# Kernel optimization log

Hardware: AMD Instinct MI355X
Metric: run time of the kernel (lower is better)

Reference implementation:

```python
import jax, jax.numpy as jnp
import numpy as np

B, S, HIDDEN = 1, 2048, 3584
NH, NKV, HD = 16, 8, 256
N_REP = NH // NKV
EPS = 1e-6
SCALING = 256.0 ** -0.5  # query_pre_attn_scalar=256
SOFTCAP = 50.0
NEG = -1e9


def rmsnorm(x, w):
    # Gemma RMSNorm with unit offset, computed in fp32
    xf = x.astype(jnp.float32)
    n = xf * jax.lax.rsqrt(jnp.mean(xf * xf, axis=-1, keepdims=True) + EPS)
    return (n * (1.0 + w.astype(jnp.float32))).astype(x.dtype)


def rope(x, cos, sin):
    # x: [B,S,H,D]; gemma pairs (x[:D/2], x[D/2:]) as complex (rotate-half)
    x1, x2 = jnp.split(x, 2, axis=-1)
    c = cos[None, :, None, :]
    s = sin[None, :, None, :]
    return jnp.concatenate([x1 * c - x2 * s, x1 * s + x2 * c], axis=-1).astype(x.dtype)


def setup_inputs() -> dict:
    key = jax.random.key(0)
    ks = jax.random.split(key, 6)
    hidden_states = jax.random.normal(ks[0], (B, S, HIDDEN), jnp.float32)
    w_qkv = jax.random.normal(ks[1], ((NH + 2 * NKV) * HD, HIDDEN), jnp.float32) * 0.02
    w_o = jax.random.normal(ks[2], (HIDDEN, NH * HD), jnp.float32) * 0.02
    q_norm_w = jax.random.normal(ks[3], (HD,), jnp.float32) * 0.1
    k_norm_w = jax.random.normal(ks[4], (HD,), jnp.float32) * 0.1
    k_cache = jnp.zeros((B, S, NKV, HD), jnp.float32)
    v_cache = jnp.zeros((B, S, NKV, HD), jnp.float32)
    kv_write_indices = jnp.arange(S, dtype=jnp.int32)
    # rotary tables, theta=10000
    inv_freq = 1.0 / (10000.0 ** (np.arange(0, HD, 2, dtype=np.float32) / HD))
    t = np.arange(S, dtype=np.float32)
    freqs = np.outer(t, inv_freq)  # [S, HD/2]
    cos = jnp.asarray(np.cos(freqs), jnp.float32)
    sin = jnp.asarray(np.sin(freqs), jnp.float32)
    # causal additive mask [1,1,S,S]
    causal = np.tril(np.ones((S, S), dtype=bool))
    mask = jnp.asarray(np.where(causal, 0.0, NEG).astype(np.float32))[None, None]
    return {"hidden_states": hidden_states, "cos": cos, "sin": sin,
            "kv_write_indices": kv_write_indices, "k_cache": k_cache,
            "v_cache": v_cache, "mask": mask, "w_qkv": w_qkv, "w_o": w_o,
            "q_norm_w": q_norm_w, "k_norm_w": k_norm_w}


def reference(hidden_states, cos, sin, kv_write_indices, k_cache, v_cache,
              mask, w_qkv, w_o, q_norm_w, k_norm_w):
    qkv = jnp.einsum('bsh,oh->bso', hidden_states, w_qkv)
    q_size, kv_size = NH * HD, NKV * HD
    xq = qkv[..., :q_size].reshape(B, S, NH, HD)
    xk = qkv[..., q_size:q_size + kv_size].reshape(B, S, NKV, HD)
    xv = qkv[..., q_size + kv_size:].reshape(B, S, NKV, HD)
    xq = rmsnorm(xq, q_norm_w)
    xk = rmsnorm(xk, k_norm_w)
    xq = rope(xq, cos, sin)
    xk = rope(xk, cos, sin)
    # KV cache write (index_copy_ along dim 1)
    kc = k_cache.at[:, kv_write_indices].set(xk)
    vc = v_cache.at[:, kv_write_indices].set(xv)
    # GQA expand
    key = jnp.repeat(kc, N_REP, axis=2)   # [B,S,NH,HD]
    val = jnp.repeat(vc, N_REP, axis=2)
    q = xq.transpose(0, 2, 1, 3) * SCALING  # [B,NH,S,HD]
    k = key.transpose(0, 2, 1, 3)
    v = val.transpose(0, 2, 1, 3)
    scores = jnp.einsum('bhqd,bhkd->bhqk', q, k)
    scores = jnp.tanh(scores / SOFTCAP) * SOFTCAP  # logit softcapping
    scores = scores + mask
    p = jax.nn.softmax(scores, axis=-1)
    out = jnp.einsum('bhqk,bhkd->bhqd', p, v)
    out = out.transpose(0, 2, 1, 3).reshape(B, S, NH * HD)
    return jnp.einsum('bsd,hd->bsh', out, w_o)
```

## Files before the change

kernel.cpp:

```cpp
#include <hip/hip_runtime.h>

typedef __bf16 bf16;
typedef __bf16 bf16x4 __attribute__((ext_vector_type(4)));
typedef __bf16 bf16x8 __attribute__((ext_vector_type(8)));
typedef float f32x4 __attribute__((ext_vector_type(4)));

#define S_LEN 2048
#define HID   3584
#define NHEADS 16
#define NKVH   8
#define HDIM   256
#define QKV_O  8192
#define O_IN   4096

typedef const __attribute__((address_space(1))) void* gp_t;
typedef __attribute__((address_space(3))) void* sp_t;

__device__ __forceinline__ void async16(const void* g, void* s) {
  __builtin_amdgcn_global_load_lds((gp_t)g, (sp_t)s, 16, 0, 0);
}

__device__ __forceinline__ f32x4 mfma16(bf16x8 a, bf16x8 b, f32x4 c) {
  return __builtin_amdgcn_mfma_f32_16x16x32_bf16(a, b, c, 0, 0, 0);
}

__global__ __launch_bounds__(256) void cast_kernel(const float* __restrict__ in,
                                                   bf16* __restrict__ out, int n4) {
  int i = blockIdx.x * 256 + threadIdx.x;
  if (i >= n4) return;
  f32x4 v = ((const f32x4*)in)[i];
  bf16x4 o = { (bf16)v[0], (bf16)v[1], (bf16)v[2], (bf16)v[3] };
  ((bf16x4*)out)[i] = o;
}

__global__ __launch_bounds__(256) void gemm_nt(const bf16* __restrict__ A, const bf16* __restrict__ B,
                                               float* __restrict__ C, int M, int N, int K) {
  __shared__ bf16 As[128 * 32];
  __shared__ bf16 Bs[128 * 32];
  int tid = threadIdx.x;
  int lane = tid & 63;
  int bm = blockIdx.y, bn = blockIdx.x;
  int w = tid >> 6, wm = w >> 1, wn = w & 1;
  int fr = lane & 15, fq = lane >> 4;
  int sr = tid >> 2;
  int scol = (tid & 3) * 8;
  const bf16* Ag = A + (size_t)(bm * 128 + sr) * K + scol;
  const bf16* Bg = B + (size_t)(bn * 128 + sr) * K + scol;
  bf16* Asl = &As[sr * 32 + scol];
  bf16* Bsl = &Bs[sr * 32 + scol];
  const bf16* Af = &As[(wm * 64 + fr) * 32 + fq * 8];
  const bf16* Bf = &Bs[(wn * 64 + fr) * 32 + fq * 8];
  f32x4 acc[4][4];
#pragma unroll
  for (int i = 0; i < 4; i++)
#pragma unroll
    for (int j = 0; j < 4; j++) { f32x4 z = {0.f, 0.f, 0.f, 0.f}; acc[i][j] = z; }
  for (int k0 = 0; k0 < K; k0 += 32) {
    __syncthreads();
    async16(Ag + k0, Asl);
    async16(Ag + (size_t)64 * K + k0, Asl + 64 * 32);
    async16(Bg + k0, Bsl);
    async16(Bg + (size_t)64 * K + k0, Bsl + 64 * 32);
    __syncthreads();
    bf16x8 a[4], b[4];
#pragma unroll
    for (int t = 0; t < 4; t++) a[t] = *(const bf16x8*)(Af + t * 16 * 32);
#pragma unroll
    for (int t = 0; t < 4; t++) b[t] = *(const bf16x8*)(Bf + t * 16 * 32);
#pragma unroll
    for (int i = 0; i < 4; i++)
#pragma unroll
      for (int j = 0; j < 4; j++) acc[i][j] = mfma16(a[i], b[j], acc[i][j]);
  }
  int row0 = bm * 128 + wm * 64 + fq * 4;
  int col0 = bn * 128 + wn * 64 + fr;
#pragma unroll
  for (int i = 0; i < 4; i++)
#pragma unroll
    for (int j = 0; j < 4; j++)
#pragma unroll
      for (int r = 0; r < 4; r++)
        C[(size_t)(row0 + i * 16 + r) * N + col0 + j * 16] = acc[i][j][r];
}

__global__ __launch_bounds__(256) void qk_norm_rope(const float* __restrict__ qkv,
                                                    const float* __restrict__ cosb,
                                                    const float* __restrict__ sinb,
                                                    const float* __restrict__ qw,
                                                    const float* __restrict__ kw,
                                                    bf16* __restrict__ qout,
                                                    bf16* __restrict__ kout) {
  int s = blockIdx.x;
  int lane = threadIdx.x & 63;
  int w = threadIdx.x >> 6;
  int d0 = lane * 4;
  int dr = d0 & 127;
  f32x4 cv = *(const f32x4*)(cosb + s * 128 + dr);
  f32x4 sv = *(const f32x4*)(sinb + s * 128 + dr);
  bool hi = lane >= 32;
#pragma unroll
  for (int r = 0; r < 6; r++) {
    int head = r * 4 + w;
    const float* x = qkv + (size_t)s * QKV_O + head * HDIM + d0;
    f32x4 v = *(const f32x4*)x;
    float ss = v[0] * v[0] + v[1] * v[1] + v[2] * v[2] + v[3] * v[3];
#pragma unroll
    for (int off = 32; off > 0; off >>= 1) ss += __shfl_xor(ss, off);
    float scale = rsqrtf(ss * (1.0f / HDIM) + 1e-6f);
    bool isq = head < NHEADS;
    const float* wn = isq ? qw : kw;
    f32x4 wv = *(const f32x4*)(wn + d0);
    float y[4], o[4];
#pragma unroll
    for (int i = 0; i < 4; i++) y[i] = v[i] * scale * (1.0f + wv[i]);
#pragma unroll
    for (int i = 0; i < 4; i++) {
      float py = __shfl_xor(y[i], 32);
      o[i] = hi ? (py * sv[i] + y[i] * cv[i]) : (y[i] * cv[i] - py * sv[i]);
    }
    float mult = isq ? 0.0625f : 1.0f;
    bf16x4 ov = { (bf16)(o[0] * mult), (bf16)(o[1] * mult), (bf16)(o[2] * mult), (bf16)(o[3] * mult) };
    if (isq) *(bf16x4*)(qout + ((size_t)head * S_LEN + s) * HDIM + d0) = ov;
    else     *(bf16x4*)(kout + ((size_t)(head - NHEADS) * S_LEN + s) * HDIM + d0) = ov;
  }
}

__global__ __launch_bounds__(256) void v_transpose(const float* __restrict__ qkv, bf16* __restrict__ vt) {
  __shared__ float tile[64][65];
  int dt = blockIdx.x, st = blockIdx.y, h = blockIdx.z;
  int t = threadIdx.x;
  int d0 = dt * 64, s0 = st * 64;
#pragma unroll
  for (int i = 0; i < 16; i++) {
    int idx = i * 256 + t;
    int r = idx >> 6, c = idx & 63;
    tile[r][c] = qkv[(size_t)(s0 + r) * QKV_O + 6144 + h * HDIM + d0 + c];
  }
  __syncthreads();
#pragma unroll
  for (int i = 0; i < 16; i++) {
    int idx = i * 256 + t;
    int dr = idx >> 6, sc = idx & 63;
    vt[((size_t)h * HDIM + d0 + dr) * S_LEN + s0 + sc] = (bf16)tile[sc][dr];
  }
}

__global__ __launch_bounds__(256) void attn_kernel(const bf16* __restrict__ q,
                                                   const bf16* __restrict__ kx,
                                                   const bf16* __restrict__ vt,
                                                   bf16* __restrict__ aout) {
  __shared__ bf16 kt[32 * 256];
  __shared__ bf16 vtile[256 * 32];
  __shared__ bf16 pbuf[4][16 * 32];
  int h = blockIdx.x, qt = blockIdx.y;
  int kvh = h >> 1;
  int tid = threadIdx.x;
  int lane = tid & 63, w = tid >> 6;
  int fr = lane & 15, fq = lane >> 4;
  int qs = qt * 64;
  bf16x8 qf[8];
  const bf16* qb = q + ((size_t)h * S_LEN + qs + w * 16 + fr) * HDIM + fq * 8;
#pragma unroll
  for (int i = 0; i < 8; i++) qf[i] = *(const bf16x8*)(qb + i * 32);
  f32x4 acc[16];
#pragma unroll
  for (int i = 0; i < 16; i++) { f32x4 z = {0.f, 0.f, 0.f, 0.f}; acc[i] = z; }
  float mrun[4] = {-1e30f, -1e30f, -1e30f, -1e30f};
  float lrun[4] = {0.f, 0.f, 0.f, 0.f};
  int krow = w * 2 + (lane >> 5);
  int kcolr = (lane & 31) * 8;
  const bf16* kg = kx + (size_t)kvh * S_LEN * HDIM;
  int vd = w * 16 + (lane >> 2);
  int vc = (lane & 3) * 8;
  const bf16* vg = vt + (size_t)kvh * HDIM * S_LEN;
  int rot0 = (fq * 8 - fr * 8) & 255;
  int rot1 = (fq * 8 - fr * 8 - 128) & 255;
  const bf16* kt0 = &kt[fr * 256];
  const bf16* kt1 = &kt[(16 + fr) * 256];
  int kmax = qs + 64;
  for (int k0 = 0; k0 < kmax; k0 += 32) {
    __syncthreads();
#pragma unroll
    for (int p = 0; p < 4; p++) {
      int r = p * 8 + krow;
      int gc = (kcolr + r * 8) & 255;
      async16(kg + (size_t)(k0 + r) * HDIM + gc, &kt[r * 256 + kcolr]);
      int d = p * 64 + vd;
      async16(vg + (size_t)d * S_LEN + k0 + vc, &vtile[d * 32 + vc]);
    }
    __syncthreads();
    f32x4 s0 = {0.f, 0.f, 0.f, 0.f}, s1 = {0.f, 0.f, 0.f, 0.f};
#pragma unroll
    for (int kk = 0; kk < 8; kk++) {
      bf16x8 b0 = *(const bf16x8*)(kt0 + ((kk * 32 + rot0) & 255));
      bf16x8 b1 = *(const bf16x8*)(kt1 + ((kk * 32 + rot1) & 255));
      s0 = mfma16(qf[kk], b0, s0);
      s1 = mfma16(qf[kk], b1, s1);
    }
    float alpha[4];
#pragma unroll
    for (int reg = 0; reg < 4; reg++) {
      int rowg = qs + w * 16 + fq * 4 + reg;
      float x0 = s0[reg], x1 = s1[reg];
      float e0 = __expf(0.04f * x0);
      float e1 = __expf(0.04f * x1);
      x0 = 50.0f * (e0 - 1.0f) / (e0 + 1.0f);
      x1 = 50.0f * (e1 - 1.0f) / (e1 + 1.0f);
      x0 = (k0 + fr <= rowg) ? x0 : -1e9f;
      x1 = (k0 + 16 + fr <= rowg) ? x1 : -1e9f;
      float mx = fmaxf(x0, x1);
      mx = fmaxf(mx, __shfl_xor(mx, 1));
      mx = fmaxf(mx, __shfl_xor(mx, 2));
      mx = fmaxf(mx, __shfl_xor(mx, 4));
      mx = fmaxf(mx, __shfl_xor(mx, 8));
      float mn = fmaxf(mrun[reg], mx);
      float a = __expf(mrun[reg] - mn);
      mrun[reg] = mn;
      float p0 = __expf(x0 - mn);
      float p1 = __expf(x1 - mn);
      float rs = p0 + p1;
      rs += __shfl_xor(rs, 1);
      rs += __shfl_xor(rs, 2);
      rs += __shfl_xor(rs, 4);
      rs += __shfl_xor(rs, 8);
      lrun[reg] = lrun[reg] * a + rs;
      alpha[reg] = a;
      pbuf[w][(fq * 4 + reg) * 32 + fr] = (bf16)p0;
      pbuf[w][(fq * 4 + reg) * 32 + 16 + fr] = (bf16)p1;
    }
#pragma unroll
    for (int ct = 0; ct < 16; ct++)
#pragma unroll
      for (int reg = 0; reg < 4; reg++) acc[ct][reg] *= alpha[reg];
    bf16x8 pf = *(const bf16x8*)&pbuf[w][fr * 32 + fq * 8];
#pragma unroll
    for (int ct = 0; ct < 16; ct++) {
      bf16x8 vf = *(const bf16x8*)&vtile[(ct * 16 + fr) * 32 + fq * 8];
      acc[ct] = mfma16(pf, vf, acc[ct]);
    }
  }
  float rl[4];
#pragma unroll
  for (int reg = 0; reg < 4; reg++) rl[reg] = 1.0f / lrun[reg];
#pragma unroll
  for (int ct = 0; ct < 16; ct++)
#pragma unroll
    for (int reg = 0; reg < 4; reg++)
      aout[(size_t)(qs + w * 16 + fq * 4 + reg) * O_IN + h * HDIM + ct * 16 + fr] =
          (bf16)(acc[ct][reg] * rl[reg]);
}

extern "C" void kernel_launch(void* const* d_in, const int* in_sizes, int n_in,
                              void* d_out, int out_size, void* d_ws, size_t ws_size,
                              hipStream_t stream) {
  const float* hidden = (const float*)d_in[0];
  const float* cosb   = (const float*)d_in[1];
  const float* sinb   = (const float*)d_in[2];
  const float* wqkv   = (const float*)d_in[7];
  const float* wo     = (const float*)d_in[8];
  const float* qnw    = (const float*)d_in[9];
  const float* knw    = (const float*)d_in[10];
  float* out = (float*)d_out;
  char* ws = (char*)d_ws;
  bf16*  h_bf    = (bf16*)(ws + 0);
  bf16*  wqkv_bf = (bf16*)(ws + 14680064);
  bf16*  wo_bf   = (bf16*)(ws + 73400320);
  float* qkv     = (float*)(ws + 102760448);
  bf16*  qb      = (bf16*)(ws + 169869312);
  bf16*  kb      = (bf16*)(ws + 186646528);
  bf16*  vtb     = (bf16*)(ws + 195035136);
  bf16*  attnb   = (bf16*)(ws + 203423744);

  cast_kernel<<<7168, 256, 0, stream>>>(hidden, h_bf, 1835008);
  cast_kernel<<<28672, 256, 0, stream>>>(wqkv, wqkv_bf, 7340032);
  cast_kernel<<<14336, 256, 0, stream>>>(wo, wo_bf, 3670016);
  gemm_nt<<<dim3(64, 16), 256, 0, stream>>>(h_bf, wqkv_bf, qkv, 2048, 8192, 3584);
  qk_norm_rope<<<2048, 256, 0, stream>>>(qkv, cosb, sinb, qnw, knw, qb, kb);
  v_transpose<<<dim3(4, 32, 8), 256, 0, stream>>>(qkv, vtb);
  attn_kernel<<<dim3(16, 32), 256, 0, stream>>>(qb, kb, vtb, attnb);
  gemm_nt<<<dim3(28, 16), 256, 0, stream>>>(attnb, wo_bf, out, 2048, 3584, 4096);
}
```

Baseline: 715.2 us.

## Use fixed softcap max in attention softmax, drop online rescaling

Because tanh softcapping bounds scores by 50, the softmax is computed as exp(s-50) directly with a fixed maximum. This removes the per-tile running max, the shuffle reductions, the alpha rescaling of the 16 accumulators, and defers the row-sum reduction to the end. It also pads the P buffer stride to reduce LDS bank conflicts and remaps query tiles so heavy and light causal tiles interleave for load balance. The risk is underflow: probabilities near exp(-100) could flush for rows whose scores are all very negative, though the causal diagonal keeps at least one valid key per row.

```diff
diff --git a/kernel.cpp b/kernel.cpp
--- a/kernel.cpp
+++ b/kernel.cpp
@@ -145,14 +145,17 @@
   }
 }
 
+#define PSTRIDE 40
 __global__ __launch_bounds__(256) void attn_kernel(const bf16* __restrict__ q,
                                                    const bf16* __restrict__ kx,
                                                    const bf16* __restrict__ vt,
                                                    bf16* __restrict__ aout) {
   __shared__ bf16 kt[32 * 256];
   __shared__ bf16 vtile[256 * 32];
-  __shared__ bf16 pbuf[4][16 * 32];
-  int h = blockIdx.x, qt = blockIdx.y;
+  __shared__ bf16 pbuf[4][16 * PSTRIDE];
+  int h = blockIdx.x;
+  int y = blockIdx.y;
+  int qt = (y < 16) ? y : 47 - y;
   int kvh = h >> 1;
   int tid = threadIdx.x;
   int lane = tid & 63, w = tid >> 6;
@@ -165,8 +168,7 @@
   f32x4 acc[16];
 #pragma unroll
   for (int i = 0; i < 16; i++) { f32x4 z = {0.f, 0.f, 0.f, 0.f}; acc[i] = z; }
-  float mrun[4] = {-1e30f, -1e30f, -1e30f, -1e30f};
-  float lrun[4] = {0.f, 0.f, 0.f, 0.f};
+  float lsum[4] = {0.f, 0.f, 0.f, 0.f};
   int krow = w * 2 + (lane >> 5);
   int kcolr = (lane & 31) * 8;
   const bf16* kg = kx + (size_t)kvh * S_LEN * HDIM;
@@ -197,42 +199,20 @@
       s0 = mfma16(qf[kk], b0, s0);
       s1 = mfma16(qf[kk], b1, s1);
     }
-    float alpha[4];
 #pragma unroll
     for (int reg = 0; reg < 4; reg++) {
       int rowg = qs + w * 16 + fq * 4 + reg;
-      float x0 = s0[reg], x1 = s1[reg];
-      float e0 = __expf(0.04f * x0);
-      float e1 = __expf(0.04f * x1);
-      x0 = 50.0f * (e0 - 1.0f) / (e0 + 1.0f);
-      x1 = 50.0f * (e1 - 1.0f) / (e1 + 1.0f);
-      x0 = (k0 + fr <= rowg) ? x0 : -1e9f;
-      x1 = (k0 + 16 + fr <= rowg) ? x1 : -1e9f;
-      float mx = fmaxf(x0, x1);
-      mx = fmaxf(mx, __shfl_xor(mx, 1));
-      mx = fmaxf(mx, __shfl_xor(mx, 2));
-      mx = fmaxf(mx, __shfl_xor(mx, 4));
-      mx = fmaxf(mx, __shfl_xor(mx, 8));
-      float mn = fmaxf(mrun[reg], mx);
-      float a = __expf(mrun[reg] - mn);
-      mrun[reg] = mn;
-      float p0 = __expf(x0 - mn);
-      float p1 = __expf(x1 - mn);
-      float rs = p0 + p1;
-      rs += __shfl_xor(rs, 1);
-      rs += __shfl_xor(rs, 2);
-      rs += __shfl_xor(rs, 4);
-      rs += __shfl_xor(rs, 8);
-      lrun[reg] = lrun[reg] * a + rs;
-      alpha[reg] = a;
-      pbuf[w][(fq * 4 + reg) * 32 + fr] = (bf16)p0;
-      pbuf[w][(fq * 4 + reg) * 32 + 16 + fr] = (bf16)p1;
-    }
-#pragma unroll
-    for (int ct = 0; ct < 16; ct++)
-#pragma unroll
-      for (int reg = 0; reg < 4; reg++) acc[ct][reg] *= alpha[reg];
-    bf16x8 pf = *(const bf16x8*)&pbuf[w][fr * 32 + fq * 8];
+      float u0 = __builtin_amdgcn_exp2f(0.057707802f * s0[reg]);
+      float u1 = __builtin_amdgcn_exp2f(0.057707802f * s1[reg]);
+      float p0 = __builtin_amdgcn_exp2f(28.853901f - 144.26950f * __builtin_amdgcn_rcpf(u0 + 1.0f));
+      float p1 = __builtin_amdgcn_exp2f(28.853901f - 144.26950f * __builtin_amdgcn_rcpf(u1 + 1.0f));
+      p0 = (k0 + fr <= rowg) ? p0 : 0.0f;
+      p1 = (k0 + 16 + fr <= rowg) ? p1 : 0.0f;
+      lsum[reg] += p0 + p1;
+      pbuf[w][(fq * 4 + reg) * PSTRIDE + fr] = (bf16)p0;
+      pbuf[w][(fq * 4 + reg) * PSTRIDE + 16 + fr] = (bf16)p1;
+    }
+    bf16x8 pf = *(const bf16x8*)&pbuf[w][fr * PSTRIDE + fq * 8];
 #pragma unroll
     for (int ct = 0; ct < 16; ct++) {
       bf16x8 vf = *(const bf16x8*)&vtile[(ct * 16 + fr) * 32 + fq * 8];
@@ -241,7 +221,14 @@
   }
   float rl[4];
 #pragma unroll
-  for (int reg = 0; reg < 4; reg++) rl[reg] = 1.0f / lrun[reg];
+  for (int reg = 0; reg < 4; reg++) {
+    float l = lsum[reg];
+    l += __shfl_xor(l, 1);
+    l += __shfl_xor(l, 2);
+    l += __shfl_xor(l, 4);
+    l += __shfl_xor(l, 8);
+    rl[reg] = 1.0f / l;
+  }
 #pragma unroll
   for (int ct = 0; ct < 16; ct++)
 #pragma unroll
```

After: 655.5 us. -8.3%, faster.
